# Performance work log

Hardware: AMD Instinct MI355X
Metric: run time of the kernel (lower is better)

The kernel has to match this reference:

```python
import jax, jax.numpy as jnp
import numpy as np

H, B, C, R, L, A, NEAR = 4, 8, 64, 64, 2048, 8, 2
EPS = 1e-5

def setup_inputs() -> dict:
    key = jax.random.key(0)
    ks = jax.random.split(key, 16)
    d = {}
    d['inputs'] = jax.random.normal(ks[0], (H, B, C, L), jnp.float32)
    d['hidden'] = jax.random.normal(ks[1], (B, R, L), jnp.float32)
    # per-head spatial attention 1x1 convs (no bias)
    d['key_w'] = jax.random.normal(ks[2], (H, R, C), jnp.float32) * 0.05
    d['value_w'] = jax.random.normal(ks[3], (H, C, C), jnp.float32) * 0.05
    # channel attention (1x1 convs with bias)
    HC = H * C
    d['ca_w1'] = jax.random.normal(ks[4], (A, HC + R), jnp.float32) * 0.05
    d['ca_b1'] = jnp.zeros((A,), jnp.float32)
    d['ca_w2'] = jax.random.normal(ks[5], (HC, A), jnp.float32) * 0.05
    d['ca_b2'] = jnp.zeros((HC,), jnp.float32)
    # projection: conv3(no bias) -> BN -> relu -> conv3(no bias) -> BN -> relu
    d['pw1'] = jax.random.normal(ks[6], (R, HC, 3), jnp.float32) * 0.02
    d['bn1_g'] = jnp.ones((R,), jnp.float32)
    d['bn1_b'] = jnp.zeros((R,), jnp.float32)
    d['bn1_m'] = jnp.zeros((R,), jnp.float32)
    d['bn1_v'] = jnp.ones((R,), jnp.float32)
    d['pw2'] = jax.random.normal(ks[7], (R, R, 3), jnp.float32) * 0.02
    d['bn2_g'] = jnp.ones((R,), jnp.float32)
    d['bn2_b'] = jnp.zeros((R,), jnp.float32)
    d['bn2_m'] = jnp.zeros((R,), jnp.float32)
    d['bn2_v'] = jnp.ones((R,), jnp.float32)
    return d

def _bn(x, g, b, m, v):
    # eval-mode BatchNorm1d over channel dim of [B,C,L]
    inv = g / jnp.sqrt(v + EPS)
    return x * inv[None, :, None] + (b - m * inv)[None, :, None]

def _conv3(x, w):
    # [B,Cin,L] x [Cout,Cin,3] -> [B,Cout,L], padding=1
    return jax.lax.conv_general_dilated(x, w, (1,), 'SAME',
                                        dimension_numbers=('NCH', 'OIH', 'NCH'))

def reference(inputs, hidden, key_w, value_w, ca_w1, ca_b1, ca_w2, ca_b2,
              pw1, bn1_g, bn1_b, bn1_m, bn1_v, pw2, bn2_g, bn2_b, bn2_m, bn2_v):
    scale = 1.0 / jnp.sqrt(jnp.float32(R))
    # spatial attention, vectorized over heads
    k = jnp.einsum('hrc,hbcl->hbrl', key_w, inputs)      # keys
    v = jnp.einsum('hoc,hbcl->hbol', value_w, inputs)    # values
    q = hidden * scale                                   # [B,R,L]
    attn = jnp.einsum('brl,hbrm->hblm', q, k)            # [H,B,L,L]
    idx = jnp.arange(L)
    band = (jnp.abs(idx[:, None] - idx[None, :]) <= NEAR).astype(attn.dtype)
    attn = jax.nn.softmax(attn * band, axis=-1)          # multiplicative mask then softmax (faithful)
    val = jnp.einsum('hbcl,hblm->hbcm', v, attn)
    enc = inputs + val                                   # dropout in eval = identity
    x = jnp.transpose(enc, (1, 0, 2, 3)).reshape(B, H * C, L)  # concat heads on channel
    # channel attention gating
    cat = jnp.concatenate([x, hidden], axis=1)           # [B,HC+R,L]
    a = jax.nn.relu(jnp.einsum('oc,bcl->bol', ca_w1, cat) + ca_b1[None, :, None])
    gate = jax.nn.sigmoid(jnp.einsum('oa,bal->bol', ca_w2, a) + ca_b2[None, :, None])
    x = x * gate
    # projection
    y = jax.nn.relu(_bn(_conv3(x, pw1), bn1_g, bn1_b, bn1_m, bn1_v))
    y = jax.nn.relu(_bn(_conv3(y, pw2), bn2_g, bn2_b, bn2_m, bn2_v))
    return y
```

## Files before the change

kernel.cpp:

```cpp
#include <hip/hip_runtime.h>
#include <hip/hip_bf16.h>
#include <math.h>

#define HH 4
#define BB 8
#define CC 64
#define RR 64
#define LL 2048
#define AA 8
#define HC 256
#define EPS 1e-5f
#define CHP 266

typedef unsigned short ushort_t;
typedef __attribute__((ext_vector_type(8))) short short8;
typedef __attribute__((ext_vector_type(4))) float f32x4;

static __device__ __forceinline__ ushort_t f2bf(float x) {
    unsigned u = __float_as_uint(x);
    unsigned r = (u + 0x7FFF + ((u >> 16) & 1)) >> 16;
    return (ushort_t)r;
}
static __device__ __forceinline__ float bf2f(ushort_t h) {
    return __uint_as_float(((unsigned)h) << 16);
}
static __device__ __forceinline__ void pack8(const float* p, short8& hi, short8& lo) {
    float4 x0 = *(const float4*)p;
    float4 x1 = *(const float4*)(p + 4);
    float xs[8] = {x0.x, x0.y, x0.z, x0.w, x1.x, x1.y, x1.z, x1.w};
#pragma unroll
    for (int e = 0; e < 8; ++e) {
        ushort_t h = f2bf(xs[e]);
        hi[e] = (short)h;
        lo[e] = (short)f2bf(xs[e] - bf2f(h));
    }
}

__global__ __launch_bounds__(256) void kABC(const float* __restrict__ inp,
                                            const float* __restrict__ kw,
                                            const float* __restrict__ vw,
                                            const float* __restrict__ hidden,
                                            float* __restrict__ XC,
                                            float* __restrict__ Spart,
                                            const float* __restrict__ pw1,
                                            const float* __restrict__ g1,
                                            const float* __restrict__ m1,
                                            const float* __restrict__ v1,
                                            const float* __restrict__ bb1,
                                            const float* __restrict__ pw2,
                                            const float* __restrict__ g2,
                                            const float* __restrict__ m2,
                                            const float* __restrict__ v2,
                                            const float* __restrict__ bb2,
                                            const float* __restrict__ w1ca,
                                            ushort_t* __restrict__ wEb,
                                            ushort_t* __restrict__ wFb,
                                            float* __restrict__ biasE,
                                            float* __restrict__ biasF,
                                            float* __restrict__ w1T) {
    if (blockIdx.x == 32) {
        int tid = blockIdx.y * 256 + threadIdx.x;
        const int stride = 32 * 256;
        for (int idx = tid; idx < 4 * 24 * 64 * 8; idx += stride) {
            int j = idx & 7, lane = (idx >> 3) & 63, t2 = idx >> 9;
            int ks = t2 % 24, rg = t2 / 24;
            int r = rg * 16 + (lane & 15);
            int k = ks * 32 + (lane >> 4) * 8 + j;
            int tap = k >> 8, ch = k & 255;
            float inv = g1[r] * rsqrtf(v1[r] + EPS);
            wEb[idx] = f2bf(pw1[(r * 256 + ch) * 3 + tap] * inv);
        }
        for (int idx = tid; idx < 4 * 6 * 64 * 8; idx += stride) {
            int j = idx & 7, lane = (idx >> 3) & 63, t2 = idx >> 9;
            int ks = t2 % 6, rg = t2 / 6;
            int r = rg * 16 + (lane & 15);
            int k = ks * 32 + (lane >> 4) * 8 + j;
            int tap = k >> 6, c = k & 63;
            float inv = g2[r] * rsqrtf(v2[r] + EPS);
            wFb[idx] = f2bf(pw2[(r * 64 + c) * 3 + tap] * inv);
        }
        for (int idx = tid; idx < 320 * 8; idx += stride)
            w1T[idx] = w1ca[(idx & 7) * 320 + (idx >> 3)];
        if (tid < 64) {
            float inv1 = g1[tid] * rsqrtf(v1[tid] + EPS);
            biasE[tid] = bb1[tid] - m1[tid] * inv1;
            float inv2 = g2[tid] * rsqrtf(v2[tid] + EPS);
            biasF[tid] = bb2[tid] - m2[tid] * inv2;
        }
        return;
    }
    int hb = blockIdx.x;
    int h = hb >> 3;
    int b = hb & 7;
    int l0 = blockIdx.y * 64;
    __shared__ __align__(16) char shbuf[2 * 80 * 72 * 2];
    ushort_t (*xsT)[80][72] = (ushort_t (*)[80][72])shbuf;
    float (*k_s)[76] = (float (*)[76])shbuf;
    __shared__ float partial[4][68][5];
    __shared__ float dw_s[68][5];
    __shared__ float u_s68[68];
    __shared__ float red_s[64];
    int t = threadIdx.x;
    int lane = t & 63, wv = t >> 6;
    int a = lane & 15, kg = lane >> 4;
    short8 ah[2][2], al[2][2];
    {
        const float* kwh = kw + h * 4096;
        const float* vwh = vw + h * 4096;
#pragma unroll
        for (int rtl = 0; rtl < 2; ++rtl) {
            int rt = wv * 2 + rtl;
            int row = rt * 16 + a;
            const float* base = (rt < 4) ? (kwh + row * 64) : (vwh + (row - 64) * 64);
#pragma unroll
            for (int ks = 0; ks < 2; ++ks)
                pack8(base + ks * 32 + kg * 8, ah[rtl][ks], al[rtl][ks]);
        }
    }
    {
        float xv[20];
#pragma unroll
        for (int it = 0; it < 20; ++it) {
            int idx = t + it * 256;
            int ch = idx / 80, j = idx % 80;
            int l = l0 - 4 + j;
            xv[it] = (j < 72 && l >= 0 && l < LL)
                   ? inp[(size_t)(hb * 64 + ch) * LL + l] : 0.f;
        }
#pragma unroll
        for (int it = 0; it < 20; ++it) {
            int idx = t + it * 256;
            int ch = idx / 80, j = idx % 80;
            ushort_t hi = f2bf(xv[it]);
            xsT[0][j][ch] = hi;
            xsT[1][j][ch] = f2bf(xv[it] - bf2f(hi));
        }
    }
    __syncthreads();
    f32x4 acc[2][5] = {};
#pragma unroll
    for (int ks = 0; ks < 2; ++ks) {
#pragma unroll
        for (int ct = 0; ct < 5; ++ct) {
            short8 bhf = *(const short8*)&xsT[0][ct * 16 + a][ks * 32 + kg * 8];
            short8 blf = *(const short8*)&xsT[1][ct * 16 + a][ks * 32 + kg * 8];
#pragma unroll
            for (int rtl = 0; rtl < 2; ++rtl) {
                acc[rtl][ct] = __builtin_amdgcn_mfma_f32_16x16x32_bf16(ah[rtl][ks], bhf, acc[rtl][ct], 0, 0, 0);
                acc[rtl][ct] = __builtin_amdgcn_mfma_f32_16x16x32_bf16(ah[rtl][ks], blf, acc[rtl][ct], 0, 0, 0);
                acc[rtl][ct] = __builtin_amdgcn_mfma_f32_16x16x32_bf16(al[rtl][ks], bhf, acc[rtl][ct], 0, 0, 0);
            }
        }
    }
    __syncthreads();
#pragma unroll
    for (int rtl = 0; rtl < 2; ++rtl) {
        int rt = wv * 2 + rtl;
        if (rt < 4) {
#pragma unroll
            for (int ct = 0; ct < 5; ++ct) {
                int j = ct * 16 + a;
#pragma unroll
                for (int reg = 0; reg < 4; ++reg) {
                    int row = rt * 16 + kg * 4 + reg;
                    if (j < 72) k_s[row][j] = acc[rtl][ct][reg];
                }
            }
        }
    }
    __syncthreads();
    {
        float acc5[5] = {};
        int l = l0 - 2 + lane;
        int lc = min(max(l, 0), LL - 1);
        const float* hp = hidden + (size_t)(b * 64 + wv * 16) * LL + lc;
#pragma unroll 4
        for (int i = 0; i < 16; ++i) {
            float hh = hp[(size_t)i * LL];
            int r = wv * 16 + i;
            acc5[0] += hh * k_s[r][lane];
            acc5[1] += hh * k_s[r][lane + 1];
            acc5[2] += hh * k_s[r][lane + 2];
            acc5[3] += hh * k_s[r][lane + 3];
            acc5[4] += hh * k_s[r][lane + 4];
        }
#pragma unroll
        for (int d = 0; d < 5; ++d) partial[wv][lane][d] = acc5[d];
        if (lane < 4) {
            int li2 = 64 + lane;
            int lb = l0 - 2 + li2;
            int lcb = min(max(lb, 0), LL - 1);
            float acc5b[5] = {};
            const float* hpb = hidden + (size_t)(b * 64 + wv * 16) * LL + lcb;
#pragma unroll 4
            for (int i = 0; i < 16; ++i) {
                float hh = hpb[(size_t)i * LL];
                int r = wv * 16 + i;
                acc5b[0] += hh * k_s[r][li2];
                acc5b[1] += hh * k_s[r][li2 + 1];
                acc5b[2] += hh * k_s[r][li2 + 2];
                acc5b[3] += hh * k_s[r][li2 + 3];
                acc5b[4] += hh * k_s[r][li2 + 4];
            }
#pragma unroll
            for (int d = 0; d < 5; ++d) partial[wv][li2][d] = acc5b[d];
        }
    }
    __syncthreads();
    if (t < 68) {
        int l = l0 - 2 + t;
        if (l < 0 || l >= LL) {
            u_s68[t] = 0.f;
#pragma unroll
            for (int d = 0; d < 5; ++d) dw_s[t][d] = 0.f;
        } else {
            float raw[5];
            float mx = 0.f;
            int nv = 0;
#pragma unroll
            for (int d = 0; d < 5; ++d) {
                float s = partial[0][t][d] + partial[1][t][d]
                        + partial[2][t][d] + partial[3][t][d];
                int m = l + d - 2;
                bool valid = (m >= 0 && m < LL);
                raw[d] = valid ? s * 0.125f : -1e30f;
                if (valid) { nv++; mx = fmaxf(mx, raw[d]); }
            }
            float e0 = __expf(-mx);
            float Z = (float)(LL - nv) * e0;
            float w[5];
#pragma unroll
            for (int d = 0; d < 5; ++d) {
                float e = (raw[d] > -1e29f) ? __expf(raw[d] - mx) : 0.f;
                w[d] = e;
                Z += e;
            }
            float inv = 1.f / Z;
            float u = e0 * inv;
            u_s68[t] = u;
#pragma unroll
            for (int d = 0; d < 5; ++d) dw_s[t][d] = w[d] * inv - u;
        }
    }
    __syncthreads();
    if (wv >= 2) {
#pragma unroll
        for (int rtl = 0; rtl < 2; ++rtl) {
            int vr0 = (wv * 2 + rtl - 4) * 16 + kg * 4;
#pragma unroll
            for (int ct = 0; ct < 5; ++ct) {
                int j = ct * 16 + a;
#pragma unroll
                for (int reg = 0; reg < 4; ++reg) {
                    if (j >= 2 && j < 70) k_s[vr0 + reg][j] = acc[rtl][ct][reg];
                }
            }
#pragma unroll
            for (int reg = 0; reg < 4; ++reg) {
                float s = 0.f;
#pragma unroll
                for (int ct = 0; ct < 5; ++ct) {
                    int j = ct * 16 + a;
                    if (j >= 4 && j < 68) s += acc[rtl][ct][reg] * u_s68[j - 2];
                }
                s += __shfl_xor(s, 1);
                s += __shfl_xor(s, 2);
                s += __shfl_xor(s, 4);
                s += __shfl_xor(s, 8);
                if (a == 0) red_s[vr0 + reg] = s;
            }
        }
    }
    __syncthreads();
    {
        int mm = t & 63;
        int cq = t >> 6;
#pragma unroll
        for (int it = 0; it < 16; ++it) {
            int c = it * 4 + cq;
            float xc = 0.f;
#pragma unroll
            for (int o = -2; o <= 2; ++o)
                xc += k_s[c][mm - o + 4] * dw_s[mm - o + 2][o + 2];
            XC[(size_t)(hb * 64 + c) * LL + l0 + mm] = xc;
        }
    }
    if (t < 64)
        Spart[((size_t)hb * 32 + blockIdx.y) * 64 + t] = red_s[t];
}

__global__ __launch_bounds__(512) void kD(const float* __restrict__ inp,
                                          const float* __restrict__ hidden,
                                          const float* __restrict__ XC,
                                          const float* __restrict__ Spart,
                                          const float* __restrict__ w1T,
                                          const float* __restrict__ b1,
                                          const float* __restrict__ w2,
                                          const float* __restrict__ b2,
                                          float* __restrict__ XG) {
    int b = blockIdx.x;
    int m0 = blockIdx.y * 64;
    __shared__ float S2_s[256];
    __shared__ float partial[8][64][9];
    int t = threadIdx.x;
    int m = t & 63;
    int wv = t >> 6;
    if (t < 256) {
        int hb = (t >> 6) * 8 + b;
        float s = 0.f;
#pragma unroll
        for (int q = 0; q < 32; ++q)
            s += Spart[((size_t)hb * 32 + q) * 64 + (t & 63)];
        S2_s[t] = s;
    }
    __syncthreads();
    float xr[4][8];
    int cb = __builtin_amdgcn_readfirstlane(wv * 8);
#pragma unroll
    for (int h = 0; h < 4; ++h) {
#pragma unroll
        for (int cc = 0; cc < 8; ++cc) {
            int c = cb + cc;
            size_t idx = (size_t)((h * 8 + b) * 64 + c) * LL + m0 + m;
            xr[h][cc] = inp[idx] + XC[idx] + S2_s[h * 64 + c];
        }
    }
    float acc2[8] = {};
#pragma unroll
    for (int h = 0; h < 4; ++h) {
#pragma unroll
        for (int cc = 0; cc < 8; ++cc) {
            const float* wp = w1T + (h * 64 + cb + cc) * 8;
            float xv = xr[h][cc];
#pragma unroll
            for (int o = 0; o < 8; ++o) acc2[o] += wp[o] * xv;
        }
    }
#pragma unroll
    for (int i = 0; i < 8; ++i) {
        const float* wp = w1T + (256 + cb + i) * 8;
        float xv = hidden[(size_t)(b * 64 + cb + i) * LL + m0 + m];
#pragma unroll
        for (int o = 0; o < 8; ++o) acc2[o] += wp[o] * xv;
    }
#pragma unroll
    for (int o = 0; o < 8; ++o) partial[wv][m][o] = acc2[o];
    __syncthreads();
    float a[8];
#pragma unroll
    for (int o = 0; o < 8; ++o) {
        float v = b1[o];
#pragma unroll
        for (int p = 0; p < 8; ++p) v += partial[p][m][o];
        a[o] = fmaxf(v, 0.f);
    }
#pragma unroll
    for (int h = 0; h < 4; ++h) {
#pragma unroll
        for (int cc = 0; cc < 8; ++cc) {
            int ch = h * 64 + cb + cc;
            const float* wp = w2 + ch * 8;
            float g = b2[ch];
#pragma unroll
            for (int o = 0; o < 8; ++o) g += wp[o] * a[o];
            float gate = 1.f / (1.f + __expf(-g));
            XG[(size_t)(b * 256 + ch) * LL + m0 + m] = xr[h][cc] * gate;
        }
    }
}

__global__ __launch_bounds__(256) void kConvM(const float* __restrict__ XG,
                                              const ushort_t* __restrict__ wEb,
                                              const float* __restrict__ biasE,
                                              float* __restrict__ Y1) {
    int b = blockIdx.x;
    int l0 = blockIdx.y * 32;
    __shared__ ushort_t xts[2][34][CHP];
    __shared__ float bias_s[64];
    int t = threadIdx.x;
    if (t < 64) bias_s[t] = biasE[t];
    for (int q = t; q < 34 * 64; q += 256) {
        int row = q % 34;
        int ch0 = (q / 34) * 4;
        int l = l0 - 1 + row;
        bool v = (l >= 0 && l < LL);
        unsigned hp[2], lp[2];
#pragma unroll
        for (int p = 0; p < 2; ++p) {
            unsigned h2 = 0, l2 = 0;
#pragma unroll
            for (int i = 0; i < 2; ++i) {
                int ch = ch0 + p * 2 + i;
                float x = v ? XG[(size_t)(b * 256 + ch) * LL + l] : 0.f;
                ushort_t hi = f2bf(x);
                ushort_t lo = f2bf(x - bf2f(hi));
                h2 |= ((unsigned)hi) << (16 * i);
                l2 |= ((unsigned)lo) << (16 * i);
            }
            hp[p] = h2; lp[p] = l2;
        }
        *(unsigned*)&xts[0][row][ch0] = hp[0];
        *(unsigned*)&xts[0][row][ch0 + 2] = hp[1];
        *(unsigned*)&xts[1][row][ch0] = lp[0];
        *(unsigned*)&xts[1][row][ch0 + 2] = lp[1];
    }
    __syncthreads();
    int lane = t & 63;
    int wid = t >> 6;
    int wm = wid & 1, wn = wid >> 1;
    int a = lane & 15;
    int kg = lane >> 4;
    f32x4 acc[2] = {};
    union U8 { unsigned u[4]; short8 s; };
#pragma unroll 4
    for (int ks = 0; ks < 24; ++ks) {
        int tap = ks >> 3;
        int ch0 = ((ks & 7) << 5) + (kg << 3);
        short8 afr[2];
#pragma unroll
        for (int tr = 0; tr < 2; ++tr) {
            const ushort_t* ap = wEb + ((((size_t)(wm * 2 + tr) * 24 + ks) * 64 + lane) << 3);
            afr[tr] = *(const short8*)ap;
        }
        int row = wn * 16 + a + tap;
        const ushort_t* xh = &xts[0][row][ch0];
        const ushort_t* xl = &xts[1][row][ch0];
        U8 bh, bl;
#pragma unroll
        for (int qq = 0; qq < 4; ++qq) {
            bh.u[qq] = *(const unsigned*)(xh + 2 * qq);
            bl.u[qq] = *(const unsigned*)(xl + 2 * qq);
        }
#pragma unroll
        for (int tr = 0; tr < 2; ++tr) {
            acc[tr] = __builtin_amdgcn_mfma_f32_16x16x32_bf16(afr[tr], bh.s, acc[tr], 0, 0, 0);
            acc[tr] = __builtin_amdgcn_mfma_f32_16x16x32_bf16(afr[tr], bl.s, acc[tr], 0, 0, 0);
        }
    }
#pragma unroll
    for (int tr = 0; tr < 2; ++tr) {
        int m = wn * 16 + a;
#pragma unroll
        for (int reg = 0; reg < 4; ++reg) {
            int r = wm * 32 + tr * 16 + kg * 4 + reg;
            float y = acc[tr][reg] + bias_s[r];
            Y1[(size_t)(b * 64 + r) * LL + l0 + m] = fmaxf(y, 0.f);
        }
    }
}

__global__ __launch_bounds__(256) void kCM2(const float* __restrict__ Y1,
                                            const ushort_t* __restrict__ wFb,
                                            const float* __restrict__ biasF,
                                            float* __restrict__ out) {
    int b = blockIdx.x;
    int l0 = blockIdx.y * 32;
    __shared__ ushort_t yts[2][34][70];
    __shared__ float bias_s[64];
    int t = threadIdx.x;
    if (t < 64) bias_s[t] = biasF[t];
    for (int q = t; q < 34 * 16; q += 256) {
        int row = q % 34;
        int c0 = (q / 34) * 4;
        int l = l0 - 1 + row;
        bool v = (l >= 0 && l < LL);
        unsigned hp[2], lp[2];
#pragma unroll
        for (int p = 0; p < 2; ++p) {
            unsigned h2 = 0, l2 = 0;
#pragma unroll
            for (int i = 0; i < 2; ++i) {
                int c = c0 + p * 2 + i;
                float x = v ? Y1[(size_t)(b * 64 + c) * LL + l] : 0.f;
                ushort_t hi = f2bf(x);
                ushort_t lo = f2bf(x - bf2f(hi));
                h2 |= ((unsigned)hi) << (16 * i);
                l2 |= ((unsigned)lo) << (16 * i);
            }
            hp[p] = h2; lp[p] = l2;
        }
        *(unsigned*)&yts[0][row][c0] = hp[0];
        *(unsigned*)&yts[0][row][c0 + 2] = hp[1];
        *(unsigned*)&yts[1][row][c0] = lp[0];
        *(unsigned*)&yts[1][row][c0 + 2] = lp[1];
    }
    __syncthreads();
    int lane = t & 63;
    int wid = t >> 6;
    int wm = wid & 1, wn = wid >> 1;
    int a = lane & 15;
    int kg = lane >> 4;
    f32x4 acc[2] = {};
    union U8 { unsigned u[4]; short8 s; };
#pragma unroll
    for (int ks = 0; ks < 6; ++ks) {
        int tap = ks >> 1;
        int c0 = ((ks & 1) << 5) + (kg << 3);
        short8 afr[2];
#pragma unroll
        for (int tr = 0; tr < 2; ++tr) {
            const ushort_t* ap = wFb + ((((size_t)(wm * 2 + tr) * 6 + ks) * 64 + lane) << 3);
            afr[tr] = *(const short8*)ap;
        }
        int s = wn * 16 + a + tap;
        const ushort_t* yh = &yts[0][s][c0];
        const ushort_t* yl = &yts[1][s][c0];
        U8 bh, bl;
#pragma unroll
        for (int qq = 0; qq < 4; ++qq) {
            bh.u[qq] = *(const unsigned*)(yh + 2 * qq);
            bl.u[qq] = *(const unsigned*)(yl + 2 * qq);
        }
#pragma unroll
        for (int tr = 0; tr < 2; ++tr) {
            acc[tr] = __builtin_amdgcn_mfma_f32_16x16x32_bf16(afr[tr], bh.s, acc[tr], 0, 0, 0);
            acc[tr] = __builtin_amdgcn_mfma_f32_16x16x32_bf16(afr[tr], bl.s, acc[tr], 0, 0, 0);
        }
    }
#pragma unroll
    for (int tr = 0; tr < 2; ++tr) {
        int m = wn * 16 + a;
#pragma unroll
        for (int reg = 0; reg < 4; ++reg) {
            int r = wm * 32 + tr * 16 + kg * 4 + reg;
            float y = acc[tr][reg] + bias_s[r];
            out[(size_t)(b * 64 + r) * LL + l0 + m] = fmaxf(y, 0.f);
        }
    }
}

extern "C" void kernel_launch(void* const* d_in, const int* in_sizes, int n_in,
                              void* d_out, int out_size, void* d_ws, size_t ws_size,
                              hipStream_t stream) {
    (void)in_sizes; (void)n_in; (void)out_size; (void)ws_size;
    const float* inp    = (const float*)d_in[0];
    const float* hidden = (const float*)d_in[1];
    const float* key_w  = (const float*)d_in[2];
    const float* value_w= (const float*)d_in[3];
    const float* ca_w1  = (const float*)d_in[4];
    const float* ca_b1  = (const float*)d_in[5];
    const float* ca_w2  = (const float*)d_in[6];
    const float* ca_b2  = (const float*)d_in[7];
    const float* pw1    = (const float*)d_in[8];
    const float* bn1_g  = (const float*)d_in[9];
    const float* bn1_b  = (const float*)d_in[10];
    const float* bn1_m  = (const float*)d_in[11];
    const float* bn1_v  = (const float*)d_in[12];
    const float* pw2    = (const float*)d_in[13];
    const float* bn2_g  = (const float*)d_in[14];
    const float* bn2_b  = (const float*)d_in[15];
    const float* bn2_m  = (const float*)d_in[16];
    const float* bn2_v  = (const float*)d_in[17];

    float* ws = (float*)d_ws;
    const size_t KV = (size_t)HH * BB * CC * LL;
    float* XG = ws;
    float* XC = ws + KV;
    float* Spart = ws + 2 * KV;
    float* w1T   = Spart + 65536;
    float* biasE = w1T + 2560;
    float* biasF = biasE + 64;
    ushort_t* wEb = (ushort_t*)(biasF + 64);
    ushort_t* wFb = (ushort_t*)(biasF + 64 + 24576);
    float* Y1 = XC;

    kABC<<<dim3(33, 32), 256, 0, stream>>>(inp, key_w, value_w, hidden,
                                           XC, Spart,
                                           pw1, bn1_g, bn1_m, bn1_v, bn1_b,
                                           pw2, bn2_g, bn2_m, bn2_v, bn2_b,
                                           ca_w1, wEb, wFb, biasE, biasF, w1T);
    kD<<<dim3(BB, LL / 64), 512, 0, stream>>>(inp, hidden, XC, Spart,
                                              w1T, ca_b1, ca_w2, ca_b2, XG);
    kConvM<<<dim3(BB, 64), 256, 0, stream>>>(XG, wEb, biasE, Y1);
    kCM2<<<dim3(BB, 64), 256, 0, stream>>>(Y1, wFb, biasF, (float*)d_out);
}
```

Before: 65.75 us.

## Halve L tiles in attention and conv1 kernels to double block count

kABC now processes 32-position tiles instead of 64, doubling the grid to 33x64, shrinking shared buffers and adding a launch-bounds occupancy hint. The Spart partial-sum layout and the reduction in kD are widened to 64 partials. kConvM uses 16-position tiles with each wave owning one 16-row output tile, doubling its grid. The aim is more blocks and better CU fill on a small problem, at the cost of a larger relative halo overhead (recomputed MFMA columns and reloaded input), more partial sums to reduce, and repeated weight loads per block.

```diff
diff --git a/kernel.cpp b/kernel.cpp
--- a/kernel.cpp
+++ b/kernel.cpp
@@ -36,31 +36,31 @@
     }
 }
 
-__global__ __launch_bounds__(256) void kABC(const float* __restrict__ inp,
-                                            const float* __restrict__ kw,
-                                            const float* __restrict__ vw,
-                                            const float* __restrict__ hidden,
-                                            float* __restrict__ XC,
-                                            float* __restrict__ Spart,
-                                            const float* __restrict__ pw1,
-                                            const float* __restrict__ g1,
-                                            const float* __restrict__ m1,
-                                            const float* __restrict__ v1,
-                                            const float* __restrict__ bb1,
-                                            const float* __restrict__ pw2,
-                                            const float* __restrict__ g2,
-                                            const float* __restrict__ m2,
-                                            const float* __restrict__ v2,
-                                            const float* __restrict__ bb2,
-                                            const float* __restrict__ w1ca,
-                                            ushort_t* __restrict__ wEb,
-                                            ushort_t* __restrict__ wFb,
-                                            float* __restrict__ biasE,
-                                            float* __restrict__ biasF,
-                                            float* __restrict__ w1T) {
+__global__ __launch_bounds__(256, 4) void kABC(const float* __restrict__ inp,
+                                               const float* __restrict__ kw,
+                                               const float* __restrict__ vw,
+                                               const float* __restrict__ hidden,
+                                               float* __restrict__ XC,
+                                               float* __restrict__ Spart,
+                                               const float* __restrict__ pw1,
+                                               const float* __restrict__ g1,
+                                               const float* __restrict__ m1,
+                                               const float* __restrict__ v1,
+                                               const float* __restrict__ bb1,
+                                               const float* __restrict__ pw2,
+                                               const float* __restrict__ g2,
+                                               const float* __restrict__ m2,
+                                               const float* __restrict__ v2,
+                                               const float* __restrict__ bb2,
+                                               const float* __restrict__ w1ca,
+                                               ushort_t* __restrict__ wEb,
+                                               ushort_t* __restrict__ wFb,
+                                               float* __restrict__ biasE,
+                                               float* __restrict__ biasF,
+                                               float* __restrict__ w1T) {
     if (blockIdx.x == 32) {
         int tid = blockIdx.y * 256 + threadIdx.x;
-        const int stride = 32 * 256;
+        const int stride = 64 * 256;
         for (int idx = tid; idx < 4 * 24 * 64 * 8; idx += stride) {
             int j = idx & 7, lane = (idx >> 3) & 63, t2 = idx >> 9;
             int ks = t2 % 24, rg = t2 / 24;
@@ -92,13 +92,13 @@
     int hb = blockIdx.x;
     int h = hb >> 3;
     int b = hb & 7;
-    int l0 = blockIdx.y * 64;
-    __shared__ __align__(16) char shbuf[2 * 80 * 72 * 2];
-    ushort_t (*xsT)[80][72] = (ushort_t (*)[80][72])shbuf;
-    float (*k_s)[76] = (float (*)[76])shbuf;
-    __shared__ float partial[4][68][5];
-    __shared__ float dw_s[68][5];
-    __shared__ float u_s68[68];
+    int l0 = blockIdx.y * 32;
+    __shared__ __align__(16) char shbuf[2 * 48 * 72 * 2];
+    ushort_t (*xsT)[48][72] = (ushort_t (*)[48][72])shbuf;
+    float (*k_s)[44] = (float (*)[44])shbuf;
+    __shared__ float partial[4][36][5];
+    __shared__ float dw_s[36][5];
+    __shared__ float u_s[36];
     __shared__ float red_s[64];
     int t = threadIdx.x;
     int lane = t & 63, wv = t >> 6;
@@ -118,30 +118,30 @@
         }
     }
     {
-        float xv[20];
-#pragma unroll
-        for (int it = 0; it < 20; ++it) {
+        float xv[12];
+#pragma unroll
+        for (int it = 0; it < 12; ++it) {
             int idx = t + it * 256;
-            int ch = idx / 80, j = idx % 80;
+            int ch = idx / 48, j = idx % 48;
             int l = l0 - 4 + j;
-            xv[it] = (j < 72 && l >= 0 && l < LL)
+            xv[it] = (j < 40 && l >= 0 && l < LL)
                    ? inp[(size_t)(hb * 64 + ch) * LL + l] : 0.f;
         }
 #pragma unroll
-        for (int it = 0; it < 20; ++it) {
+        for (int it = 0; it < 12; ++it) {
             int idx = t + it * 256;
-            int ch = idx / 80, j = idx % 80;
+            int ch = idx / 48, j = idx % 48;
             ushort_t hi = f2bf(xv[it]);
             xsT[0][j][ch] = hi;
             xsT[1][j][ch] = f2bf(xv[it] - bf2f(hi));
         }
     }
     __syncthreads();
-    f32x4 acc[2][5] = {};
+    f32x4 acc[2][3] = {};
 #pragma unroll
     for (int ks = 0; ks < 2; ++ks) {
 #pragma unroll
-        for (int ct = 0; ct < 5; ++ct) {
+        for (int ct = 0; ct < 3; ++ct) {
             short8 bhf = *(const short8*)&xsT[0][ct * 16 + a][ks * 32 + kg * 8];
             short8 blf = *(const short8*)&xsT[1][ct * 16 + a][ks * 32 + kg * 8];
 #pragma unroll
@@ -158,18 +158,18 @@
         int rt = wv * 2 + rtl;
         if (rt < 4) {
 #pragma unroll
-            for (int ct = 0; ct < 5; ++ct) {
+            for (int ct = 0; ct < 3; ++ct) {
                 int j = ct * 16 + a;
 #pragma unroll
                 for (int reg = 0; reg < 4; ++reg) {
                     int row = rt * 16 + kg * 4 + reg;
-                    if (j < 72) k_s[row][j] = acc[rtl][ct][reg];
+                    if (j < 44) k_s[row][j] = acc[rtl][ct][reg];
                 }
             }
         }
     }
     __syncthreads();
-    {
+    if (lane < 36) {
         float acc5[5] = {};
         int l = l0 - 2 + lane;
         int lc = min(max(l, 0), LL - 1);
@@ -186,31 +186,12 @@
         }
 #pragma unroll
         for (int d = 0; d < 5; ++d) partial[wv][lane][d] = acc5[d];
-        if (lane < 4) {
-            int li2 = 64 + lane;
-            int lb = l0 - 2 + li2;
-            int lcb = min(max(lb, 0), LL - 1);
-            float acc5b[5] = {};
-            const float* hpb = hidden + (size_t)(b * 64 + wv * 16) * LL + lcb;
-#pragma unroll 4
-            for (int i = 0; i < 16; ++i) {
-                float hh = hpb[(size_t)i * LL];
-                int r = wv * 16 + i;
-                acc5b[0] += hh * k_s[r][li2];
-                acc5b[1] += hh * k_s[r][li2 + 1];
-                acc5b[2] += hh * k_s[r][li2 + 2];
-                acc5b[3] += hh * k_s[r][li2 + 3];
-                acc5b[4] += hh * k_s[r][li2 + 4];
-            }
-#pragma unroll
-            for (int d = 0; d < 5; ++d) partial[wv][li2][d] = acc5b[d];
-        }
-    }
-    __syncthreads();
-    if (t < 68) {
+    }
+    __syncthreads();
+    if (t < 36) {
         int l = l0 - 2 + t;
         if (l < 0 || l >= LL) {
-            u_s68[t] = 0.f;
+            u_s[t] = 0.f;
 #pragma unroll
             for (int d = 0; d < 5; ++d) dw_s[t][d] = 0.f;
         } else {
@@ -237,7 +218,7 @@
             }
             float inv = 1.f / Z;
             float u = e0 * inv;
-            u_s68[t] = u;
+            u_s[t] = u;
 #pragma unroll
             for (int d = 0; d < 5; ++d) dw_s[t][d] = w[d] * inv - u;
         }
@@ -248,20 +229,20 @@
         for (int rtl = 0; rtl < 2; ++rtl) {
             int vr0 = (wv * 2 + rtl - 4) * 16 + kg * 4;
 #pragma unroll
-            for (int ct = 0; ct < 5; ++ct) {
+            for (int ct = 0; ct < 3; ++ct) {
                 int j = ct * 16 + a;
 #pragma unroll
                 for (int reg = 0; reg < 4; ++reg) {
-                    if (j >= 2 && j < 70) k_s[vr0 + reg][j] = acc[rtl][ct][reg];
+                    if (j >= 2 && j < 38) k_s[vr0 + reg][j] = acc[rtl][ct][reg];
                 }
             }
 #pragma unroll
             for (int reg = 0; reg < 4; ++reg) {
                 float s = 0.f;
 #pragma unroll
-                for (int ct = 0; ct < 5; ++ct) {
+                for (int ct = 0; ct < 3; ++ct) {
                     int j = ct * 16 + a;
-                    if (j >= 4 && j < 68) s += acc[rtl][ct][reg] * u_s68[j - 2];
+                    if (j >= 4 && j < 36) s += acc[rtl][ct][reg] * u_s[j - 2];
                 }
                 s += __shfl_xor(s, 1);
                 s += __shfl_xor(s, 2);
@@ -273,11 +254,11 @@
     }
     __syncthreads();
     {
-        int mm = t & 63;
-        int cq = t >> 6;
-#pragma unroll
-        for (int it = 0; it < 16; ++it) {
-            int c = it * 4 + cq;
+        int mm = t & 31;
+        int cq = t >> 5;
+#pragma unroll
+        for (int it = 0; it < 8; ++it) {
+            int c = it * 8 + cq;
             float xc = 0.f;
 #pragma unroll
             for (int o = -2; o <= 2; ++o)
@@ -286,7 +267,7 @@
         }
     }
     if (t < 64)
-        Spart[((size_t)hb * 32 + blockIdx.y) * 64 + t] = red_s[t];
+        Spart[((size_t)hb * 64 + blockIdx.y) * 64 + t] = red_s[t];
 }
 
 __global__ __launch_bounds__(512) void kD(const float* __restrict__ inp,
@@ -309,8 +290,8 @@
         int hb = (t >> 6) * 8 + b;
         float s = 0.f;
 #pragma unroll
-        for (int q = 0; q < 32; ++q)
-            s += Spart[((size_t)hb * 32 + q) * 64 + (t & 63)];
+        for (int q = 0; q < 64; ++q)
+            s += Spart[((size_t)hb * 64 + q) * 64 + (t & 63)];
         S2_s[t] = s;
     }
     __syncthreads();
@@ -374,14 +355,14 @@
                                               const float* __restrict__ biasE,
                                               float* __restrict__ Y1) {
     int b = blockIdx.x;
-    int l0 = blockIdx.y * 32;
-    __shared__ ushort_t xts[2][34][CHP];
+    int l0 = blockIdx.y * 16;
+    __shared__ ushort_t xts[2][18][CHP];
     __shared__ float bias_s[64];
     int t = threadIdx.x;
     if (t < 64) bias_s[t] = biasE[t];
-    for (int q = t; q < 34 * 64; q += 256) {
-        int row = q % 34;
-        int ch0 = (q / 34) * 4;
+    for (int q = t; q < 18 * 64; q += 256) {
+        int row = q % 18;
+        int ch0 = (q / 18) * 4;
         int l = l0 - 1 + row;
         bool v = (l >= 0 && l < LL);
         unsigned hp[2], lp[2];
@@ -407,22 +388,17 @@
     __syncthreads();
     int lane = t & 63;
     int wid = t >> 6;
-    int wm = wid & 1, wn = wid >> 1;
     int a = lane & 15;
     int kg = lane >> 4;
-    f32x4 acc[2] = {};
+    f32x4 acc = {};
     union U8 { unsigned u[4]; short8 s; };
 #pragma unroll 4
     for (int ks = 0; ks < 24; ++ks) {
         int tap = ks >> 3;
         int ch0 = ((ks & 7) << 5) + (kg << 3);
-        short8 afr[2];
-#pragma unroll
-        for (int tr = 0; tr < 2; ++tr) {
-            const ushort_t* ap = wEb + ((((size_t)(wm * 2 + tr) * 24 + ks) * 64 + lane) << 3);
-            afr[tr] = *(const short8*)ap;
-        }
-        int row = wn * 16 + a + tap;
+        const ushort_t* ap = wEb + ((((size_t)wid * 24 + ks) * 64 + lane) << 3);
+        short8 afr = *(const short8*)ap;
+        int row = a + tap;
         const ushort_t* xh = &xts[0][row][ch0];
         const ushort_t* xl = &xts[1][row][ch0];
         U8 bh, bl;
@@ -431,19 +407,15 @@
             bh.u[qq] = *(const unsigned*)(xh + 2 * qq);
             bl.u[qq] = *(const unsigned*)(xl + 2 * qq);
         }
-#pragma unroll
-        for (int tr = 0; tr < 2; ++tr) {
-            acc[tr] = __builtin_amdgcn_mfma_f32_16x16x32_bf16(afr[tr], bh.s, acc[tr], 0, 0, 0);
-            acc[tr] = __builtin_amdgcn_mfma_f32_16x16x32_bf16(afr[tr], bl.s, acc[tr], 0, 0, 0);
-        }
-    }
-#pragma unroll
-    for (int tr = 0; tr < 2; ++tr) {
-        int m = wn * 16 + a;
+        acc = __builtin_amdgcn_mfma_f32_16x16x32_bf16(afr, bh.s, acc, 0, 0, 0);
+        acc = __builtin_amdgcn_mfma_f32_16x16x32_bf16(afr, bl.s, acc, 0, 0, 0);
+    }
+    {
+        int m = a;
 #pragma unroll
         for (int reg = 0; reg < 4; ++reg) {
-            int r = wm * 32 + tr * 16 + kg * 4 + reg;
-            float y = acc[tr][reg] + bias_s[r];
+            int r = wid * 16 + kg * 4 + reg;
+            float y = acc[reg] + bias_s[r];
             Y1[(size_t)(b * 64 + r) * LL + l0 + m] = fmaxf(y, 0.f);
         }
     }
@@ -557,20 +529,20 @@
     float* XG = ws;
     float* XC = ws + KV;
     float* Spart = ws + 2 * KV;
-    float* w1T   = Spart + 65536;
+    float* w1T   = Spart + 131072;
     float* biasE = w1T + 2560;
     float* biasF = biasE + 64;
     ushort_t* wEb = (ushort_t*)(biasF + 64);
     ushort_t* wFb = (ushort_t*)(biasF + 64 + 24576);
     float* Y1 = XC;
 
-    kABC<<<dim3(33, 32), 256, 0, stream>>>(inp, key_w, value_w, hidden,
+    kABC<<<dim3(33, 64), 256, 0, stream>>>(inp, key_w, value_w, hidden,
                                            XC, Spart,
                                            pw1, bn1_g, bn1_m, bn1_v, bn1_b,
                                            pw2, bn2_g, bn2_m, bn2_v, bn2_b,
                                            ca_w1, wEb, wFb, biasE, biasF, w1T);
     kD<<<dim3(BB, LL / 64), 512, 0, stream>>>(inp, hidden, XC, Spart,
                                               w1T, ca_b1, ca_w2, ca_b2, XG);
-    kConvM<<<dim3(BB, 64), 256, 0, stream>>>(XG, wEb, biasE, Y1);
+    kConvM<<<dim3(BB, 128), 256, 0, stream>>>(XG, wEb, biasE, Y1);
     kCM2<<<dim3(BB, 64), 256, 0, stream>>>(Y1, wFb, biasF, (float*)d_out);
 }
```

After: 64.82 us. Within noise of the previous version (-1.4%).
